# Kernel tuning notes

Measured on AMD Instinct MI355X. Metric: run time of the kernel, lower is better.

The kernel has to match this reference:

```python
import jax, jax.numpy as jnp
import numpy as np

D_ORIG, D_HEAD, N_HEAD = 64, 32, 8
D_EMB = D_HEAD * N_HEAD


def setup_inputs() -> dict:
    key = jax.random.key(0)
    ks = jax.random.split(key, 9)
    b, l = 1, 512
    x = jax.random.normal(ks[0], (b, l, D_ORIG), dtype=jnp.float32)
    e = jax.random.normal(ks[1], (b, l, l, D_ORIG), dtype=jnp.float32)
    s = 1.0 / np.sqrt(D_ORIG)
    Wq = jax.random.uniform(ks[2], (D_ORIG, D_EMB), jnp.float32, -s, s)
    Wk = jax.random.uniform(ks[3], (D_ORIG, D_EMB), jnp.float32, -s, s)
    Wv = jax.random.uniform(ks[4], (D_ORIG, D_EMB), jnp.float32, -s, s)
    We = jax.random.uniform(ks[5], (D_ORIG, D_EMB), jnp.float32, -s, s)
    so = 1.0 / np.sqrt(D_EMB)
    Wo = jax.random.uniform(ks[6], (D_EMB, D_ORIG), jnp.float32, -so, so)
    bo = jax.random.uniform(ks[7], (D_ORIG,), jnp.float32, -so, so)
    return {"x": x, "e": e, "Wq": Wq, "Wk": Wk, "Wv": Wv, "We": We, "Wo": Wo, "bo": bo}


def reference(x, e, Wq, Wk, Wv, We, Wo, bo):
    b, l, _ = x.shape
    # projections
    q = (x @ Wq).reshape(b, l, N_HEAD, D_HEAD).transpose(0, 2, 1, 3)  # b n l d
    k = (x @ Wk).reshape(b, l, N_HEAD, D_HEAD).transpose(0, 2, 1, 3)
    v = (x @ Wv).reshape(b, l, N_HEAD, D_HEAD).transpose(0, 2, 1, 3)
    ee = (e @ We).reshape(b, l, l, N_HEAD, D_HEAD).transpose(0, 3, 1, 2, 4)  # b n i j d
    # edge-biased keys/values: broadcast add over query index i
    kb = k[:, :, None, :, :] + ee  # b n i j d
    logit = jnp.einsum('bnid,bnijd->bnij', q, kb) * (D_HEAD ** -0.5)
    attn = jax.nn.softmax(logit, axis=-1)
    vb = v[:, :, None, :, :] + ee  # b n i j d
    out = jnp.einsum('bnij,bnijd->bnid', attn, vb)  # b n i d
    out = out.transpose(0, 2, 1, 3).reshape(b, l, D_EMB)
    return out @ Wo + bo
```

## Files before the change

### kernel.cpp

```cpp
#include <hip/hip_runtime.h>

#define SCALE 0.17677669529663687f
#define PSTR 513

__global__ __launch_bounds__(512, 4) void fused_kernel(
    const float* __restrict__ e, const float* __restrict__ x,
    const float* __restrict__ Wq, const float* __restrict__ Wk,
    const float* __restrict__ We, const float* __restrict__ Wv,
    const float* __restrict__ Wo, const float* __restrict__ bo,
    float* __restrict__ out) {
  const int t = threadIdx.x, i = blockIdx.x;
  __shared__ float s_x[64];
  __shared__ __align__(16) float s_q[256];
  __shared__ __align__(16) float s_qc[1024];
  __shared__ __align__(16) float s_p[8 * PSTR];
  __shared__ __align__(16) float s_pt[512 * 8];
  __shared__ __align__(16) float s_part[8 * 1024];
  __shared__ float s_ae[512], s_px[512];
  __shared__ float s_emb[256];
  __shared__ float s_op[8 * 64];

  if (t < 64) s_x[t] = x[i * 64 + t];
  __syncthreads();
  if (t < 256) {
    float a = 0;
#pragma unroll 8
    for (int c = 0; c < 64; ++c) a += s_x[c] * Wq[c * 256 + t];
    s_q[t] = a * SCALE;
  }
  __syncthreads();
  {
    const int c = t >> 3, h = t & 7;
    const float4* wer = (const float4*)(We + c * 256 + h * 32);
    const float4* wkr = (const float4*)(Wk + c * 256 + h * 32);
    const float4* qr = (const float4*)(s_q + h * 32);
    float se = 0, sk = 0;
#pragma unroll
    for (int u = 0; u < 8; ++u) {
      float4 w1 = wer[u], w2 = wkr[u], qv = qr[u];
      se += qv.x * w1.x + qv.y * w1.y + qv.z * w1.z + qv.w * w1.w;
      sk += qv.x * w2.x + qv.y * w2.y + qv.z * w2.z + qv.w * w2.w;
    }
    s_qc[c * 16 + h] = se;
    s_qc[c * 16 + 8 + h] = sk;
  }
  __syncthreads();

  {
    const int j = t;
    const float4* erow = (const float4*)(e + (size_t)(i * 512 + j) * 64);
    const float4* xrow = (const float4*)(x + j * 64);
    float acc[8];
#pragma unroll
    for (int h = 0; h < 8; ++h) acc[h] = 0.f;
#pragma unroll 4
    for (int c4 = 0; c4 < 16; ++c4) {
      float4 E = erow[c4];
      float4 X = xrow[c4];
      const float* qc = s_qc + c4 * 64;
#pragma unroll
      for (int h = 0; h < 8; ++h) {
        acc[h] += E.x * qc[h]      + E.y * qc[16 + h]
                + E.z * qc[32 + h] + E.w * qc[48 + h]
                + X.x * qc[8 + h]  + X.y * qc[24 + h]
                + X.z * qc[40 + h] + X.w * qc[56 + h];
      }
    }
#pragma unroll
    for (int h = 0; h < 8; ++h) s_p[h * PSTR + j] = acc[h];
  }
  __syncthreads();

  {
    const int n = t >> 6, l64 = t & 63;
    float m = -1e30f;
#pragma unroll
    for (int u = 0; u < 8; ++u) m = fmaxf(m, s_p[n * PSTR + l64 + u * 64]);
#pragma unroll
    for (int off = 32; off; off >>= 1) m = fmaxf(m, __shfl_xor(m, off, 64));
    float pv[8];
    float sum = 0;
#pragma unroll
    for (int u = 0; u < 8; ++u) {
      pv[u] = __expf(s_p[n * PSTR + l64 + u * 64] - m);
      sum += pv[u];
    }
#pragma unroll
    for (int off = 32; off; off >>= 1) sum += __shfl_xor(sum, off, 64);
    const float inv = 1.0f / sum;
#pragma unroll
    for (int u = 0; u < 8; ++u) s_pt[(l64 + u * 64) * 8 + n] = pv[u] * inv;
  }
  __syncthreads();

  {
    const int lane = t & 63, w = t >> 6;
    float ae[8], px[8];
#pragma unroll
    for (int h = 0; h < 8; ++h) { ae[h] = 0.f; px[h] = 0.f; }
    const float* ep = e + (size_t)i * 32768 + (size_t)w * 4096 + lane;
    const float* xp = x + w * 4096 + lane;
#pragma unroll 4
    for (int jj = 0; jj < 64; ++jj) {
      const int j = w * 64 + jj;
      float ev = ep[jj * 64];
      float xv = xp[jj * 64];
      const float4* pt = (const float4*)(s_pt + j * 8);
      float4 p0 = pt[0], p1 = pt[1];
      ae[0] += p0.x * ev; ae[1] += p0.y * ev; ae[2] += p0.z * ev; ae[3] += p0.w * ev;
      ae[4] += p1.x * ev; ae[5] += p1.y * ev; ae[6] += p1.z * ev; ae[7] += p1.w * ev;
      px[0] += p0.x * xv; px[1] += p0.y * xv; px[2] += p0.z * xv; px[3] += p0.w * xv;
      px[4] += p1.x * xv; px[5] += p1.y * xv; px[6] += p1.z * xv; px[7] += p1.w * xv;
    }
#pragma unroll
    for (int h = 0; h < 8; ++h) {
      s_part[w * 1024 + h * 64 + lane] = ae[h];
      s_part[w * 1024 + 512 + h * 64 + lane] = px[h];
    }
  }
  __syncthreads();

  {
    float va = 0, vp = 0;
#pragma unroll
    for (int w = 0; w < 8; ++w) {
      va += s_part[w * 1024 + t];
      vp += s_part[w * 1024 + 512 + t];
    }
    s_ae[t] = va; s_px[t] = vp;
  }
  __syncthreads();

  {
    const int nd = t & 255, ch = t >> 8, hn = nd >> 5;
    float emb = 0;
    const int cb = ch * 32;
#pragma unroll 8
    for (int c = cb; c < cb + 32; ++c)
      emb += s_ae[hn * 64 + c] * We[c * 256 + nd] + s_px[hn * 64 + c] * Wv[c * 256 + nd];
    s_part[ch * 256 + nd] = emb;
  }
  __syncthreads();
  if (t < 256) s_emb[t] = s_part[t] + s_part[256 + t];
  __syncthreads();
  {
    const int o = t & 63, mc = t >> 6;
    float oo = 0;
#pragma unroll 8
    for (int m2 = mc * 32; m2 < mc * 32 + 32; ++m2) oo += s_emb[m2] * Wo[m2 * 64 + o];
    s_op[mc * 64 + o] = oo;
  }
  __syncthreads();
  if (t < 64) {
    float r = bo[t];
#pragma unroll
    for (int w = 0; w < 8; ++w) r += s_op[w * 64 + t];
    out[i * 64 + t] = r;
  }
}

extern "C" void kernel_launch(void* const* d_in, const int* in_sizes, int n_in,
                              void* d_out, int out_size, void* d_ws, size_t ws_size,
                              hipStream_t stream) {
  const float* x  = (const float*)d_in[0];
  const float* e  = (const float*)d_in[1];
  const float* Wq = (const float*)d_in[2];
  const float* Wk = (const float*)d_in[3];
  const float* Wv = (const float*)d_in[4];
  const float* We = (const float*)d_in[5];
  const float* Wo = (const float*)d_in[6];
  const float* bo = (const float*)d_in[7];
  float* out = (float*)d_out;

  hipLaunchKernelGGL(fused_kernel, dim3(512), dim3(512), 0, stream,
                     e, x, Wq, Wk, We, Wv, Wo, bo, out);
}
```

Before: 139.9 us.

## Prefetch edge rows into registers and drop transposed probability buffer

```diff
diff --git a/kernel.cpp b/kernel.cpp
--- a/kernel.cpp
+++ b/kernel.cpp
@@ -1,7 +1,18 @@
 #include <hip/hip_runtime.h>
 
 #define SCALE 0.17677669529663687f
-#define PSTR 513
+#define PSTR 516
+
+#define FMA64(E, X, qc)                                                         \
+  {                                                                             \
+    const float* _q = (qc);                                                     \
+    _Pragma("unroll")                                                           \
+    for (int h = 0; h < 8; ++h)                                                 \
+      acc[h] += (E).x * _q[h]      + (E).y * _q[16 + h]                         \
+              + (E).z * _q[32 + h] + (E).w * _q[48 + h]                         \
+              + (X).x * _q[8 + h]  + (X).y * _q[24 + h]                         \
+              + (X).z * _q[40 + h] + (X).w * _q[56 + h];                        \
+  }
 
 __global__ __launch_bounds__(512, 4) void fused_kernel(
     const float* __restrict__ e, const float* __restrict__ x,
@@ -14,7 +25,6 @@
   __shared__ __align__(16) float s_q[256];
   __shared__ __align__(16) float s_qc[1024];
   __shared__ __align__(16) float s_p[8 * PSTR];
-  __shared__ __align__(16) float s_pt[512 * 8];
   __shared__ __align__(16) float s_part[8 * 1024];
   __shared__ float s_ae[512], s_px[512];
   __shared__ float s_emb[256];
@@ -50,22 +60,22 @@
     const int j = t;
     const float4* erow = (const float4*)(e + (size_t)(i * 512 + j) * 64);
     const float4* xrow = (const float4*)(x + j * 64);
+    float4 Eb[8], Xb[8];
+#pragma unroll
+    for (int u = 0; u < 8; ++u) Eb[u] = erow[u];
+#pragma unroll
+    for (int u = 0; u < 8; ++u) Xb[u] = xrow[u];
     float acc[8];
 #pragma unroll
     for (int h = 0; h < 8; ++h) acc[h] = 0.f;
-#pragma unroll 4
-    for (int c4 = 0; c4 < 16; ++c4) {
-      float4 E = erow[c4];
-      float4 X = xrow[c4];
-      const float* qc = s_qc + c4 * 64;
 #pragma unroll
-      for (int h = 0; h < 8; ++h) {
-        acc[h] += E.x * qc[h]      + E.y * qc[16 + h]
-                + E.z * qc[32 + h] + E.w * qc[48 + h]
-                + X.x * qc[8 + h]  + X.y * qc[24 + h]
-                + X.z * qc[40 + h] + X.w * qc[56 + h];
-      }
+    for (int u = 0; u < 8; ++u) {
+      FMA64(Eb[u], Xb[u], s_qc + u * 64);
+      Eb[u] = erow[8 + u];
+      Xb[u] = xrow[8 + u];
     }
+#pragma unroll
+    for (int u = 0; u < 8; ++u) FMA64(Eb[u], Xb[u], s_qc + (8 + u) * 64);
 #pragma unroll
     for (int h = 0; h < 8; ++h) s_p[h * PSTR + j] = acc[h];
   }
@@ -89,7 +99,7 @@
     for (int off = 32; off; off >>= 1) sum += __shfl_xor(sum, off, 64);
     const float inv = 1.0f / sum;
 #pragma unroll
-    for (int u = 0; u < 8; ++u) s_pt[(l64 + u * 64) * 8 + n] = pv[u] * inv;
+    for (int u = 0; u < 8; ++u) s_p[n * PSTR + l64 + u * 64] = pv[u] * inv;
   }
   __syncthreads();
 
@@ -100,17 +110,22 @@
     for (int h = 0; h < 8; ++h) { ae[h] = 0.f; px[h] = 0.f; }
     const float* ep = e + (size_t)i * 32768 + (size_t)w * 4096 + lane;
     const float* xp = x + w * 4096 + lane;
-#pragma unroll 4
-    for (int jj = 0; jj < 64; ++jj) {
-      const int j = w * 64 + jj;
-      float ev = ep[jj * 64];
-      float xv = xp[jj * 64];
-      const float4* pt = (const float4*)(s_pt + j * 8);
-      float4 p0 = pt[0], p1 = pt[1];
-      ae[0] += p0.x * ev; ae[1] += p0.y * ev; ae[2] += p0.z * ev; ae[3] += p0.w * ev;
-      ae[4] += p1.x * ev; ae[5] += p1.y * ev; ae[6] += p1.z * ev; ae[7] += p1.w * ev;
-      px[0] += p0.x * xv; px[1] += p0.y * xv; px[2] += p0.z * xv; px[3] += p0.w * xv;
-      px[4] += p1.x * xv; px[5] += p1.y * xv; px[6] += p1.z * xv; px[7] += p1.w * xv;
+    for (int jb = 0; jb < 64; jb += 8) {
+      float ev[8], xv[8];
+#pragma unroll
+      for (int u = 0; u < 8; ++u) ev[u] = ep[(jb + u) * 64];
+#pragma unroll
+      for (int u = 0; u < 8; ++u) xv[u] = xp[(jb + u) * 64];
+      const int j0 = w * 64 + jb;
+#pragma unroll
+      for (int h = 0; h < 8; ++h) {
+        float4 pa = *(const float4*)&s_p[h * PSTR + j0];
+        float4 pb = *(const float4*)&s_p[h * PSTR + j0 + 4];
+        ae[h] += pa.x * ev[0] + pa.y * ev[1] + pa.z * ev[2] + pa.w * ev[3]
+               + pb.x * ev[4] + pb.y * ev[5] + pb.z * ev[6] + pb.w * ev[7];
+        px[h] += pa.x * xv[0] + pa.y * xv[1] + pa.z * xv[2] + pa.w * xv[3]
+               + pb.x * xv[4] + pb.y * xv[5] + pb.z * xv[6] + pb.w * xv[7];
+      }
     }
 #pragma unroll
     for (int h = 0; h < 8; ++h) {
```

Result: slower. 143.7 us (+2.7%).

## Stream e through double-buffered LDS tiles with online softmax in one pass

Applied to the files above, without the earlier changes.

```diff
diff --git a/kernel.cpp b/kernel.cpp
--- a/kernel.cpp
+++ b/kernel.cpp
@@ -1,7 +1,7 @@
 #include <hip/hip_runtime.h>
 
 #define SCALE 0.17677669529663687f
-#define PSTR 513
+#define BSTR 68
 
 __global__ __launch_bounds__(512, 4) void fused_kernel(
     const float* __restrict__ e, const float* __restrict__ x,
@@ -10,127 +10,164 @@
     const float* __restrict__ Wo, const float* __restrict__ bo,
     float* __restrict__ out) {
   const int t = threadIdx.x, i = blockIdx.x;
-  __shared__ float s_x[64];
-  __shared__ __align__(16) float s_q[256];
-  __shared__ __align__(16) float s_qc[1024];
-  __shared__ __align__(16) float s_p[8 * PSTR];
-  __shared__ __align__(16) float s_pt[512 * 8];
-  __shared__ __align__(16) float s_part[8 * 1024];
-  __shared__ float s_ae[512], s_px[512];
-  __shared__ float s_emb[256];
-  __shared__ float s_op[8 * 64];
-
-  if (t < 64) s_x[t] = x[i * 64 + t];
-  __syncthreads();
+  const int wv = t >> 6, lane = t & 63;
+  const int js = t >> 3, g = t & 7, c8 = g * 8;
+
+  __shared__ __align__(16) float sm[12304];
+  float* bufs  = sm;
+  float* qch   = sm + 8704;
+  float* s_pl  = sm + 9728;
+  float* s_al  = sm + 10496;
+  float* s_l   = sm + 10504;
+  float* s_ae  = sm + 10512;
+  float* s_px  = sm + 11024;
+  float* s_emb = sm + 11536;
+  float* s_op  = sm + 11792;
+  float* s_part = sm;
+
+  const float* gbase = e + ((size_t)i << 15);
+
+  float4 stA = *(const float4*)(gbase + js * 64 + c8);
+  float4 stB = *(const float4*)(gbase + js * 64 + c8 + 4);
+
   if (t < 256) {
+    const float* xr = x + i * 64;
     float a = 0;
 #pragma unroll 8
-    for (int c = 0; c < 64; ++c) a += s_x[c] * Wq[c * 256 + t];
-    s_q[t] = a * SCALE;
-  }
-  __syncthreads();
-  {
-    const int c = t >> 3, h = t & 7;
-    const float4* wer = (const float4*)(We + c * 256 + h * 32);
-    const float4* wkr = (const float4*)(Wk + c * 256 + h * 32);
-    const float4* qr = (const float4*)(s_q + h * 32);
+    for (int c = 0; c < 64; ++c) a += xr[c] * Wq[c * 256 + t];
+    s_pl[(t & 31) * 8 + (t >> 5)] = a * SCALE;
+  }
+  __syncthreads();
+
+  {
+    const float4* wer = (const float4*)(We + js * 256 + g * 32);
+    const float4* wkr = (const float4*)(Wk + js * 256 + g * 32);
     float se = 0, sk = 0;
 #pragma unroll
-    for (int u = 0; u < 8; ++u) {
-      float4 w1 = wer[u], w2 = wkr[u], qv = qr[u];
-      se += qv.x * w1.x + qv.y * w1.y + qv.z * w1.z + qv.w * w1.w;
-      sk += qv.x * w2.x + qv.y * w2.y + qv.z * w2.z + qv.w * w2.w;
-    }
-    s_qc[c * 16 + h] = se;
-    s_qc[c * 16 + 8 + h] = sk;
-  }
-  __syncthreads();
-
-  {
-    const int j = t;
-    const float4* erow = (const float4*)(e + (size_t)(i * 512 + j) * 64);
-    const float4* xrow = (const float4*)(x + j * 64);
-    float acc[8];
-#pragma unroll
-    for (int h = 0; h < 8; ++h) acc[h] = 0.f;
-#pragma unroll 4
-    for (int c4 = 0; c4 < 16; ++c4) {
-      float4 E = erow[c4];
-      float4 X = xrow[c4];
-      const float* qc = s_qc + c4 * 64;
+    for (int d4 = 0; d4 < 8; ++d4) {
+      float4 w1 = wer[d4], w2 = wkr[d4];
+      float q0 = s_pl[(d4 * 4 + 0) * 8 + g], q1 = s_pl[(d4 * 4 + 1) * 8 + g];
+      float q2 = s_pl[(d4 * 4 + 2) * 8 + g], q3 = s_pl[(d4 * 4 + 3) * 8 + g];
+      se += q0 * w1.x + q1 * w1.y + q2 * w1.z + q3 * w1.w;
+      sk += q0 * w2.x + q1 * w2.y + q2 * w2.z + q3 * w2.w;
+    }
+    qch[g * 64 + js] = se;
+    qch[512 + g * 64 + js] = sk;
+  }
+  {
+    float* wb = bufs + js * BSTR + c8;
+    *(float4*)wb = stA;
+    *(float4*)(wb + 4) = stB;
+  }
+  stA = *(const float4*)(gbase + ((64 + js) << 6) + c8);
+  stB = *(const float4*)(gbase + ((64 + js) << 6) + c8 + 4);
+  __syncthreads();
+
+  float m_run = -1e30f, l_run = 0.f;
+  float ae[8], px[8];
+#pragma unroll
+  for (int h = 0; h < 8; ++h) { ae[h] = 0.f; px[h] = 0.f; }
+
+  for (int k = 0; k < 8; ++k) {
+    const float* buf = bufs + (k & 1) * (64 * BSTR);
+    float* nbuf = bufs + ((k & 1) ^ 1) * (64 * BSTR);
+
+    {
+      const float* xr = x + ((k * 64 + js) << 6) + c8;
+      float4 xa = *(const float4*)xr;
+      float4 xb = *(const float4*)(xr + 4);
+      const float* er = buf + js * BSTR + c8;
+      float4 ea = *(const float4*)er;
+      float4 eb = *(const float4*)(er + 4);
+      float acc[8];
 #pragma unroll
       for (int h = 0; h < 8; ++h) {
-        acc[h] += E.x * qc[h]      + E.y * qc[16 + h]
-                + E.z * qc[32 + h] + E.w * qc[48 + h]
-                + X.x * qc[8 + h]  + X.y * qc[24 + h]
-                + X.z * qc[40 + h] + X.w * qc[56 + h];
+        const float4* ce = (const float4*)(qch + h * 64 + c8);
+        const float4* cx = (const float4*)(qch + 512 + h * 64 + c8);
+        float4 c0 = ce[0], c1 = ce[1], d0 = cx[0], d1 = cx[1];
+        acc[h] = ea.x * c0.x + ea.y * c0.y + ea.z * c0.z + ea.w * c0.w
+               + eb.x * c1.x + eb.y * c1.y + eb.z * c1.z + eb.w * c1.w
+               + xa.x * d0.x + xa.y * d0.y + xa.z * d0.z + xa.w * d0.w
+               + xb.x * d1.x + xb.y * d1.y + xb.z * d1.z + xb.w * d1.w;
       }
-    }
-#pragma unroll
-    for (int h = 0; h < 8; ++h) s_p[h * PSTR + j] = acc[h];
-  }
-  __syncthreads();
-
-  {
-    const int n = t >> 6, l64 = t & 63;
-    float m = -1e30f;
-#pragma unroll
-    for (int u = 0; u < 8; ++u) m = fmaxf(m, s_p[n * PSTR + l64 + u * 64]);
-#pragma unroll
-    for (int off = 32; off; off >>= 1) m = fmaxf(m, __shfl_xor(m, off, 64));
-    float pv[8];
-    float sum = 0;
-#pragma unroll
-    for (int u = 0; u < 8; ++u) {
-      pv[u] = __expf(s_p[n * PSTR + l64 + u * 64] - m);
-      sum += pv[u];
-    }
-#pragma unroll
-    for (int off = 32; off; off >>= 1) sum += __shfl_xor(sum, off, 64);
-    const float inv = 1.0f / sum;
-#pragma unroll
-    for (int u = 0; u < 8; ++u) s_pt[(l64 + u * 64) * 8 + n] = pv[u] * inv;
-  }
-  __syncthreads();
-
-  {
-    const int lane = t & 63, w = t >> 6;
-    float ae[8], px[8];
-#pragma unroll
-    for (int h = 0; h < 8; ++h) { ae[h] = 0.f; px[h] = 0.f; }
-    const float* ep = e + (size_t)i * 32768 + (size_t)w * 4096 + lane;
-    const float* xp = x + w * 4096 + lane;
-#pragma unroll 4
-    for (int jj = 0; jj < 64; ++jj) {
-      const int j = w * 64 + jj;
-      float ev = ep[jj * 64];
-      float xv = xp[jj * 64];
-      const float4* pt = (const float4*)(s_pt + j * 8);
-      float4 p0 = pt[0], p1 = pt[1];
-      ae[0] += p0.x * ev; ae[1] += p0.y * ev; ae[2] += p0.z * ev; ae[3] += p0.w * ev;
-      ae[4] += p1.x * ev; ae[5] += p1.y * ev; ae[6] += p1.z * ev; ae[7] += p1.w * ev;
-      px[0] += p0.x * xv; px[1] += p0.y * xv; px[2] += p0.z * xv; px[3] += p0.w * xv;
-      px[4] += p1.x * xv; px[5] += p1.y * xv; px[6] += p1.z * xv; px[7] += p1.w * xv;
-    }
-#pragma unroll
-    for (int h = 0; h < 8; ++h) {
-      s_part[w * 1024 + h * 64 + lane] = ae[h];
-      s_part[w * 1024 + 512 + h * 64 + lane] = px[h];
-    }
-  }
-  __syncthreads();
-
-  {
+#pragma unroll
+      for (int m = 1; m <= 4; m <<= 1)
+#pragma unroll
+        for (int h = 0; h < 8; ++h) acc[h] += __shfl_xor(acc[h], m, 64);
+      if (g == 0) {
+        *(float4*)(s_pl + js * 12) = make_float4(acc[0], acc[1], acc[2], acc[3]);
+        *(float4*)(s_pl + js * 12 + 4) = make_float4(acc[4], acc[5], acc[6], acc[7]);
+      }
+    }
+    __syncthreads();
+
+    {
+      float lg = s_pl[lane * 12 + wv];
+      float cm = lg;
+#pragma unroll
+      for (int off = 32; off; off >>= 1) cm = fmaxf(cm, __shfl_xor(cm, off, 64));
+      float mnew = fmaxf(m_run, cm);
+      float al = __expf(m_run - mnew);
+      float p = __expf(lg - mnew);
+      float ss = p;
+#pragma unroll
+      for (int off = 32; off; off >>= 1) ss += __shfl_xor(ss, off, 64);
+      l_run = l_run * al + ss;
+      m_run = mnew;
+      s_pl[lane * 12 + wv] = p;
+      if (lane == 0) s_al[wv] = al;
+    }
+    if (k < 7) {
+      float* wb = nbuf + js * BSTR + c8;
+      *(float4*)wb = stA;
+      *(float4*)(wb + 4) = stB;
+    }
+    if (k < 6) {
+      const float* gs = gbase + ((((k + 2) << 6) + js) << 6) + c8;
+      stA = *(const float4*)gs;
+      stB = *(const float4*)(gs + 4);
+    }
+    __syncthreads();
+
+    {
+#pragma unroll
+      for (int h = 0; h < 8; ++h) { float a_ = s_al[h]; ae[h] *= a_; px[h] *= a_; }
+      const float* xc = x + (k << 12) + lane;
+#pragma unroll
+      for (int u = 0; u < 8; ++u) {
+        const int jj = (wv << 3) + u;
+        float ev = buf[jj * BSTR + lane];
+        float xv = xc[jj << 6];
+        float4 p0 = *(const float4*)(s_pl + jj * 12);
+        float4 p1 = *(const float4*)(s_pl + jj * 12 + 4);
+        ae[0] += p0.x * ev; ae[1] += p0.y * ev; ae[2] += p0.z * ev; ae[3] += p0.w * ev;
+        ae[4] += p1.x * ev; ae[5] += p1.y * ev; ae[6] += p1.z * ev; ae[7] += p1.w * ev;
+        px[0] += p0.x * xv; px[1] += p0.y * xv; px[2] += p0.z * xv; px[3] += p0.w * xv;
+        px[4] += p1.x * xv; px[5] += p1.y * xv; px[6] += p1.z * xv; px[7] += p1.w * xv;
+      }
+    }
+    __syncthreads();
+  }
+
+  if (lane == 0) s_l[wv] = l_run;
+#pragma unroll
+  for (int h = 0; h < 8; ++h) {
+    s_part[wv * 1024 + h * 64 + lane] = ae[h];
+    s_part[wv * 1024 + 512 + h * 64 + lane] = px[h];
+  }
+  __syncthreads();
+  {
+    const float inv = 1.0f / s_l[t >> 6];
     float va = 0, vp = 0;
 #pragma unroll
     for (int w = 0; w < 8; ++w) {
       va += s_part[w * 1024 + t];
       vp += s_part[w * 1024 + 512 + t];
     }
-    s_ae[t] = va; s_px[t] = vp;
-  }
-  __syncthreads();
-
+    s_ae[t] = va * inv;
+    s_px[t] = vp * inv;
+  }
+  __syncthreads();
   {
     const int nd = t & 255, ch = t >> 8, hn = nd >> 5;
     float emb = 0;
```

Measured after the change: 160.1 us. 1.14x slower.
